# Performance work log

Measured on AMD Instinct MI355X. Metric: run time of the kernel, lower is better.

The kernel has to match this reference:

```python
import jax, jax.numpy as jnp
import numpy as np

BN_EPS = 1e-5
NUM_ROUTING_ITERS = 3


def _bn(x, gamma, beta, axes):
    # training-mode batch norm (torch default train mode): batch statistics
    mean = x.mean(axes, keepdims=True)
    var = x.var(axes, keepdims=True)
    return (x - mean) * jax.lax.rsqrt(var + BN_EPS) * gamma + beta


def _squash(x):
    # squash over last dim: sn * x / ((1+sn) * sqrt(sn))
    sn = jnp.sum(x * x, axis=-1, keepdims=True)
    return sn * x / ((1.0 + sn) * jnp.sqrt(sn))


def setup_inputs() -> dict:
    key = jax.random.key(0)
    ks = jax.random.split(key, 16)
    B, N = 4, 2048          # batch, num_points
    P, Q = 1024, 16         # prim_caps_size, prim_vec_size
    L, V = 64, 64           # latent_caps_size, latent_vec_size
    OUT = 40
    s = 0.02
    return {
        "x": jax.random.normal(ks[0], (B, 3, N), dtype=jnp.float32),
        # ConvLayer
        "w1": jax.random.normal(ks[1], (64, 3), dtype=jnp.float32) * s,
        "b1": jnp.zeros((64,), jnp.float32),
        "g1": jnp.ones((64,), jnp.float32),
        "be1": jnp.zeros((64,), jnp.float32),
        "w2": jax.random.normal(ks[2], (128, 64), dtype=jnp.float32) * s,
        "b2": jnp.zeros((128,), jnp.float32),
        "g2": jnp.ones((128,), jnp.float32),
        "be2": jnp.zeros((128,), jnp.float32),
        # PrimaryPointCapsLayer: Q parallel conv1d(128->P, k=1)+BN branches, stacked
        "w3": jax.random.normal(ks[3], (Q, P, 128), dtype=jnp.float32) * s,
        "b3": jnp.zeros((Q, P), jnp.float32),
        "g3": jnp.ones((Q, P), jnp.float32),
        "be3": jnp.zeros((Q, P), jnp.float32),
        # LatentCapsLayer routing weights
        "Wr": jax.random.normal(ks[4], (L, P, V, Q), dtype=jnp.float32) * 0.01,
        # classifier head
        "fc_w": jax.random.normal(ks[5], (OUT, L * V), dtype=jnp.float32) * s,
        "fc_b": jnp.zeros((OUT,), jnp.float32),
    }


def reference(x, w1, b1, g1, be1, w2, b2, g2, be2, w3, b3, g3, be3, Wr, fc_w, fc_b):
    B = x.shape[0]
    # ConvLayer: two 1x1 conv1d + BN + ReLU
    h = jnp.einsum("oc,bcn->bon", w1, x) + b1[None, :, None]
    h = jax.nn.relu(_bn(h, g1[None, :, None], be1[None, :, None], (0, 2)))
    h = jnp.einsum("oc,bcn->bon", w2, h) + b2[None, :, None]
    h = jax.nn.relu(_bn(h, g2[None, :, None], be2[None, :, None], (0, 2)))  # [B,128,N]

    # PrimaryPointCapsLayer: Q branches of conv1d+BN+global maxpool, vectorized
    u = jnp.einsum("qpc,bcn->bqpn", w3, h) + b3[None, :, :, None]  # [B,Q,P,N]
    u = _bn(u, g3[None, :, :, None], be3[None, :, :, None], (0, 3))
    u = u.max(axis=-1)                      # global maxpool -> [B,Q,P]
    u = jnp.transpose(u, (0, 2, 1))         # stack dim=2 in torch -> [B,P,Q]
    u = _squash(u)                          # squash over prim_vec

    # LatentCapsLayer dynamic routing
    u_hat = jnp.einsum("lpvq,bpq->blpv", Wr, u)   # [B,L,P,V]
    u_hat_d = jax.lax.stop_gradient(u_hat)
    L, P = Wr.shape[0], Wr.shape[1]
    b_ij = jnp.zeros((B, L, P), u_hat.dtype)
    for _ in range(NUM_ROUTING_ITERS - 1):
        c_ij = jax.nn.softmax(b_ij, axis=1)
        v_j = _squash(jnp.einsum("blp,blpv->blv", c_ij, u_hat_d))
        b_ij = b_ij + jnp.einsum("blv,blpv->blp", v_j, u_hat_d)
    c_ij = jax.nn.softmax(b_ij, axis=1)
    v_j = _squash(jnp.einsum("blp,blpv->blv", c_ij, u_hat))  # [B,L,V]

    presence = jnp.linalg.norm(v_j, axis=2)                   # [B,L]
    logits = v_j.reshape(B, -1) @ fc_w.T + fc_b               # [B,OUT]
    return (logits, presence)
```

## Files before the change

### kernel.cpp

```cpp
#include <hip/hip_runtime.h>
#include <math.h>

#define BN_EPS 1e-5f

typedef __attribute__((ext_vector_type(8))) _Float16 half8;
typedef __attribute__((ext_vector_type(4))) _Float16 half4;
typedef __attribute__((ext_vector_type(4))) float f32x4;
#define SPLIT_S  2048.0f
#define INV_S    (1.0f/2048.0f)

__global__ __launch_bounds__(256) void k_conv1stats(const float* __restrict__ x,
        const float* __restrict__ w1, float* __restrict__ y1,
        float* __restrict__ mean, float* __restrict__ inv) {
    const int o = blockIdx.x, t = threadIdx.x;
    const float wa = w1[o*3+0], wb = w1[o*3+1], wc = w1[o*3+2];
    float s = 0.f, ss = 0.f;
#pragma unroll
    for (int it = 0; it < 8; ++it) {
        int i = it * 256 + t;
        int b = i >> 9, n4 = (i & 511) * 4;
        const float* xb = x + (size_t)b * 6144 + n4;
        float4 x0 = *(const float4*)(xb);
        float4 x1 = *(const float4*)(xb + 2048);
        float4 x2 = *(const float4*)(xb + 4096);
        float4 r;
        r.x = wa*x0.x + wb*x1.x + wc*x2.x;
        r.y = wa*x0.y + wb*x1.y + wc*x2.y;
        r.z = wa*x0.z + wb*x1.z + wc*x2.z;
        r.w = wa*x0.w + wb*x1.w + wc*x2.w;
        *(float4*)(y1 + o * 8192 + i * 4) = r;
        s += r.x + r.y + r.z + r.w;
        ss = fmaf(r.x, r.x, fmaf(r.y, r.y, fmaf(r.z, r.z, fmaf(r.w, r.w, ss))));
    }
    __shared__ float rs[256], rss[256];
    rs[t] = s; rss[t] = ss;
    __syncthreads();
    for (int off = 128; off > 0; off >>= 1) {
        if (t < off) { rs[t] += rs[t+off]; rss[t] += rss[t+off]; }
        __syncthreads();
    }
    if (t == 0) {
        float m = rs[0] * (1.f/8192.f);
        float var = rss[0] * (1.f/8192.f) - m*m;
        mean[o] = m;
        inv[o]  = rsqrtf(var + BN_EPS);
    }
}

__global__ void k_stats(const float* __restrict__ y, float* __restrict__ mean,
                        float* __restrict__ inv) {
    int c = blockIdx.x, t = threadIdx.x;
    float s = 0.f, ss = 0.f;
    const float4* src = (const float4*)(y + c * 8192);
    for (int i = t; i < 2048; i += 256) {
        float4 v = src[i];
        s += v.x + v.y + v.z + v.w;
        ss = fmaf(v.x, v.x, fmaf(v.y, v.y, fmaf(v.z, v.z, fmaf(v.w, v.w, ss))));
    }
    __shared__ float rs[256], rss[256];
    rs[t] = s; rss[t] = ss;
    __syncthreads();
    for (int off = 128; off > 0; off >>= 1) {
        if (t < off) { rs[t] += rs[t+off]; rss[t] += rss[t+off]; }
        __syncthreads();
    }
    if (t == 0) {
        float m = rs[0] * (1.f/8192.f);
        float var = rss[0] * (1.f/8192.f) - m*m;
        mean[c] = m;
        inv[c]  = rsqrtf(var + BN_EPS);
    }
}

__global__ __launch_bounds__(256) void k_conv2(const float* __restrict__ y1,
        const float* __restrict__ w2,
        const float* __restrict__ mean1, const float* __restrict__ inv1,
        const float* __restrict__ g1, const float* __restrict__ be1,
        float* __restrict__ y2) {
    __shared__ float sc1[64], sh1[64];
    const int t = threadIdx.x;
    if (t < 64) {
        float sc = inv1[t] * g1[t];
        sc1[t] = sc;
        sh1[t] = be1[t] - mean1[t] * sc;
    }
    __syncthreads();
    int bn0 = (blockIdx.x * 256 + t) * 4;
    int og0 = blockIdx.y * 4;
    float4 acc[4];
#pragma unroll
    for (int j = 0; j < 4; ++j) acc[j] = float4{0.f,0.f,0.f,0.f};
    for (int c = 0; c < 64; ++c) {
        float4 hv = *(const float4*)(y1 + c*8192 + bn0);
        float sc = sc1[c], sh = sh1[c];
        hv.x = fmaxf(fmaf(hv.x, sc, sh), 0.f);
        hv.y = fmaxf(fmaf(hv.y, sc, sh), 0.f);
        hv.z = fmaxf(fmaf(hv.z, sc, sh), 0.f);
        hv.w = fmaxf(fmaf(hv.w, sc, sh), 0.f);
#pragma unroll
        for (int j = 0; j < 4; ++j) {
            float w = w2[(og0+j)*64 + c];
            acc[j].x = fmaf(w, hv.x, acc[j].x); acc[j].y = fmaf(w, hv.y, acc[j].y);
            acc[j].z = fmaf(w, hv.z, acc[j].z); acc[j].w = fmaf(w, hv.w, acc[j].w);
        }
    }
#pragma unroll
    for (int j = 0; j < 4; ++j) *(float4*)(y2 + (og0+j)*8192 + bn0) = acc[j];
}

__global__ void k_split_w3(const float* __restrict__ w, const float* __restrict__ g3,
                           _Float16* __restrict__ hi, _Float16* __restrict__ lo) {
    int base = blockIdx.x * 256 + threadIdx.x;
#pragma unroll
    for (int it = 0; it < 4; ++it) {
        int i = (base + it * 131072) * 4;
        float4 d = *reinterpret_cast<const float4*>(w + i);
        float sgn = (g3[i >> 7] < 0.f) ? -1.f : 1.f;
        float vs[4] = {d.x * sgn, d.y * sgn, d.z * sgn, d.w * sgn};
        half4 h4, l4;
#pragma unroll
        for (int j = 0; j < 4; ++j) {
            _Float16 h = (_Float16)vs[j];
            h4[j] = h;
            l4[j] = (_Float16)((vs[j] - (float)h) * SPLIT_S);
        }
        *reinterpret_cast<half4*>(hi + i) = h4;
        *reinterpret_cast<half4*>(lo + i) = l4;
    }
}

__global__ __launch_bounds__(256) void k_h2t_split(const float* __restrict__ y2,
        const float* __restrict__ mean, const float* __restrict__ inv,
        const float* __restrict__ g, const float* __restrict__ be,
        _Float16* __restrict__ hi, _Float16* __restrict__ lo) {
    __shared__ float tile[64][65];
    const int t = threadIdx.x;
    const int bn0 = blockIdx.x * 64, c0 = blockIdx.y * 64;
#pragma unroll
    for (int r = 0; r < 4; ++r) {
        int idx = r * 256 + t;
        int cl = idx >> 4, bn4 = (idx & 15) * 4;
        int c = c0 + cl;
        float sc = inv[c] * g[c];
        float sh = be[c] - mean[c] * sc;
        float4 d = *(const float4*)(y2 + (size_t)c * 8192 + bn0 + bn4);
        tile[cl][bn4  ] = fmaxf(fmaf(d.x, sc, sh), 0.f);
        tile[cl][bn4+1] = fmaxf(fmaf(d.y, sc, sh), 0.f);
        tile[cl][bn4+2] = fmaxf(fmaf(d.z, sc, sh), 0.f);
        tile[cl][bn4+3] = fmaxf(fmaf(d.w, sc, sh), 0.f);
    }
    __syncthreads();
#pragma unroll
    for (int r = 0; r < 4; ++r) {
        int idx = r * 256 + t;
        int bnl = idx >> 4, c4 = (idx & 15) * 4;
        half4 h4, l4;
#pragma unroll
        for (int j = 0; j < 4; ++j) {
            float v = tile[c4 + j][bnl];
            _Float16 h = (_Float16)v;
            h4[j] = h;
            l4[j] = (_Float16)((v - (float)h) * SPLIT_S);
        }
        size_t o = (size_t)(bn0 + bnl) * 128 + c0 + c4;
        *reinterpret_cast<half4*>(hi + o) = h4;
        *reinterpret_cast<half4*>(lo + o) = l4;
    }
}

__global__ __launch_bounds__(256, 2) void k_caps(
        const _Float16* __restrict__ w3h, const _Float16* __restrict__ w3l,
        const _Float16* __restrict__ h2h, const _Float16* __restrict__ h2l,
        float* __restrict__ umax,
        float* __restrict__ usum_b, float* __restrict__ usumsq_b) {
    const int lane = threadIdx.x & 63, wave = threadIdx.x >> 6;
    const int b = blockIdx.y;
    const int mrow = blockIdx.x * 128 + wave * 32;
    const int r16 = lane & 15, kq = lane >> 4;

    __shared__ _Float16 Bs[2][2][8][64][8];

    half8 Ah[2][4], Al[2][4];
#pragma unroll
    for (int mt = 0; mt < 2; ++mt) {
        const size_t base = (size_t)(mrow + mt*16 + r16) * 128 + kq * 8;
#pragma unroll
        for (int ks = 0; ks < 4; ++ks) {
            Ah[mt][ks] = *reinterpret_cast<const half8*>(w3h + base + ks*32);
            Al[mt][ks] = *reinterpret_cast<const half8*>(w3l + base + ks*32);
        }
    }
    float mx[2][4], sm[2][4], sq[2][4];
#pragma unroll
    for (int mt = 0; mt < 2; ++mt)
#pragma unroll
        for (int r = 0; r < 4; ++r) {
            mx[mt][r] = -3.4e38f; sm[mt][r] = 0.f; sq[mt][r] = 0.f;
        }

    const int u0 = wave * 2;
    const size_t srow = (size_t)(b*2048 + r16) * 128 + wave * 32 + kq * 8;

    {
#pragma unroll
        for (int g = 0; g < 2; ++g) {
            const size_t a = srow + (size_t)g * 16 * 128;
            *reinterpret_cast<half8*>(&Bs[0][g][u0  ][lane][0]) = *reinterpret_cast<const half8*>(h2h + a);
            *reinterpret_cast<half8*>(&Bs[0][g][u0+1][lane][0]) = *reinterpret_cast<const half8*>(h2l + a);
        }
    }
    __syncthreads();

    for (int nt = 0; nt < 64; ++nt) {
        const int buf = nt & 1;
        const int ntn = (nt + 1 < 64) ? nt + 1 : nt;
        const size_t snext = srow + (size_t)ntn * 32 * 128;
        half8 g0h = *reinterpret_cast<const half8*>(h2h + snext);
        half8 g0l = *reinterpret_cast<const half8*>(h2l + snext);
        half8 g1h = *reinterpret_cast<const half8*>(h2h + snext + 2048);
        half8 g1l = *reinterpret_cast<const half8*>(h2l + snext + 2048);

#pragma unroll
        for (int g = 0; g < 2; ++g) {
            f32x4 acc[2], accx[2];
#pragma unroll
            for (int mt = 0; mt < 2; ++mt) { acc[mt] = f32x4{0.f,0.f,0.f,0.f}; accx[mt] = f32x4{0.f,0.f,0.f,0.f}; }
#pragma unroll
            for (int ks = 0; ks < 4; ++ks) {
                half8 Bh = *reinterpret_cast<const half8*>(&Bs[buf][g][ks*2  ][lane][0]);
                half8 Bl = *reinterpret_cast<const half8*>(&Bs[buf][g][ks*2+1][lane][0]);
#pragma unroll
                for (int mt = 0; mt < 2; ++mt) {
                    acc[mt]  = __builtin_amdgcn_mfma_f32_16x16x32_f16(Ah[mt][ks], Bh, acc[mt], 0, 0, 0);
                    accx[mt] = __builtin_amdgcn_mfma_f32_16x16x32_f16(Ah[mt][ks], Bl, accx[mt], 0, 0, 0);
                    accx[mt] = __builtin_amdgcn_mfma_f32_16x16x32_f16(Al[mt][ks], Bh, accx[mt], 0, 0, 0);
                }
            }
#pragma unroll
            for (int mt = 0; mt < 2; ++mt)
#pragma unroll
                for (int r = 0; r < 4; ++r) {
                    float v = fmaf(accx[mt][r], INV_S, acc[mt][r]);
                    mx[mt][r] = fmaxf(mx[mt][r], v);
                    sm[mt][r] += v;
                    sq[mt][r] = fmaf(v, v, sq[mt][r]);
                }
        }
        *reinterpret_cast<half8*>(&Bs[buf^1][0][u0  ][lane][0]) = g0h;
        *reinterpret_cast<half8*>(&Bs[buf^1][0][u0+1][lane][0]) = g0l;
        *reinterpret_cast<half8*>(&Bs[buf^1][1][u0  ][lane][0]) = g1h;
        *reinterpret_cast<half8*>(&Bs[buf^1][1][u0+1][lane][0]) = g1l;
        __syncthreads();
    }

#pragma unroll
    for (int off = 8; off >= 1; off >>= 1)
#pragma unroll
        for (int mt = 0; mt < 2; ++mt)
#pragma unroll
            for (int r = 0; r < 4; ++r) {
                mx[mt][r] = fmaxf(mx[mt][r], __shfl_xor(mx[mt][r], off));
                sm[mt][r] += __shfl_xor(sm[mt][r], off);
                sq[mt][r] += __shfl_xor(sq[mt][r], off);
            }
    if (r16 == 0) {
#pragma unroll
        for (int mt = 0; mt < 2; ++mt)
#pragma unroll
            for (int r = 0; r < 4; ++r) {
                int qp = mrow + mt*16 + kq*4 + r;
                umax[b*16384 + qp]     = mx[mt][r];
                usum_b[b*16384 + qp]   = sm[mt][r];
                usumsq_b[b*16384 + qp] = sq[mt][r];
            }
    }
}

__global__ void k_u(const float* __restrict__ umax,
                    const float* __restrict__ usum_b, const float* __restrict__ usumsq_b,
                    const float* __restrict__ g3, const float* __restrict__ be3,
                    float* __restrict__ u) {
    int tg = blockIdx.x * 256 + threadIdx.x;
    int b = tg >> 10, p = tg & 1023;
    float ub[16]; float sn = 0.f;
#pragma unroll
    for (int q = 0; q < 16; ++q) {
        int qp = q * 1024 + p;
        float s  = usum_b[qp] + usum_b[16384+qp] + usum_b[32768+qp] + usum_b[49152+qp];
        float ss = usumsq_b[qp] + usumsq_b[16384+qp] + usumsq_b[32768+qp] + usumsq_b[49152+qp];
        float g  = g3[qp];
        float sgn = (g < 0.f) ? -1.f : 1.f;
        float mean  = sgn * s * (1.f/8192.f);
        float var   = ss * (1.f/8192.f) - mean*mean;
        float scale = g * rsqrtf(var + BN_EPS);
        float val = sgn * umax[b*16384 + qp];
        float vb = (val - mean) * scale + be3[qp];
        ub[q] = vb; sn = fmaf(vb, vb, sn);
    }
    float f = sqrtf(sn) / (1.f + sn);
#pragma unroll
    for (int q = 0; q < 16; ++q) u[tg*16 + q] = ub[q] * f;
}

__global__ __launch_bounds__(256) void k_uhat(const float* __restrict__ Wr,
                                              const float* __restrict__ u,
                                              float* __restrict__ uhat2,
                                              float* __restrict__ s1p) {
    const int t = threadIdx.x;
    const int pblk = blockIdx.x, l = blockIdx.y;
    __shared__ float wr[4][64][20];
    __shared__ float us[4][4][16];
    const int bb = t >> 6, v = t & 63;
    float s1acc = 0.f;
    for (int sub = 0; sub < 8; ++sub) {
        const int p0 = pblk * 32 + sub * 4;
        const float* src = Wr + ((size_t)l * 1024 + p0) * 1024;
        if (sub) __syncthreads();
#pragma unroll
        for (int it = 0; it < 4; ++it) {
            float4 d = *(const float4*)(src + (it*256 + t) * 4);
            int vv = t >> 2, q0 = (t & 3) * 4;
            *(float4*)&wr[it][vv][q0] = d;
        }
        {
            int p = t >> 6, b2 = (t >> 4) & 3, q = t & 15;
            us[p][b2][q] = u[((size_t)b2 * 1024 + p0 + p) * 16 + q];
        }
        __syncthreads();
#pragma unroll
        for (int p = 0; p < 4; ++p) {
            float acc = 0.f;
#pragma unroll
            for (int q4 = 0; q4 < 4; ++q4) {
                float4 wf = *(const float4*)&wr[p][v][q4*4];
                float4 uf = *(const float4*)&us[p][bb][q4*4];
                acc = fmaf(wf.x, uf.x, acc);
                acc = fmaf(wf.y, uf.y, acc);
                acc = fmaf(wf.z, uf.z, acc);
                acc = fmaf(wf.w, uf.w, acc);
            }
            uhat2[(((size_t)bb * 1024 + p0 + p) * 64 + l) * 64 + v] = acc;
            s1acc += acc;
        }
    }
    s1p[(((size_t)pblk * 4 + bb) * 64 + l) * 64 + v] = s1acc;
}

__global__ void k_s1red(const float* __restrict__ s1p, float* __restrict__ vout) {
    const int wv = blockIdx.x;
    const int b = wv >> 6, l = wv & 63;
    const int v = threadIdx.x;
    float acc = 0.f;
#pragma unroll
    for (int pblk = 0; pblk < 32; ++pblk)
        acc += s1p[(((size_t)pblk * 4 + b) * 64 + l) * 64 + v];
    float s = acc * (1.f/64.f);
    float sn = s * s;
#pragma unroll
    for (int off = 32; off >= 1; off >>= 1) sn += __shfl_xor(sn, off);
    vout[wv * 64 + v] = s * sqrtf(sn) / (1.f + sn);
}

__global__ __launch_bounds__(256) void k_route(const float* __restrict__ uhat2,
                                               const float* __restrict__ vin,
                                               float* __restrict__ bij,
                                               float* __restrict__ part, const int read_b) {
    const int blk = blockIdx.x;
    const int b = blk >> 7, ch = blk & 127;
    const int p0 = ch * 8;
    const int t = threadIdx.x;
    const int v = t & 63, w = t >> 6;
    __shared__ float uh[64][68];
    __shared__ float vs[64][68];
    __shared__ float bl[64];
    {
        const float* src = vin + b * 4096;
        for (int i = t; i < 1024; i += 256) {
            float4 d = *(const float4*)(src + i * 4);
            int l = i >> 4, v0 = (i & 15) * 4;
            vs[l][v0] = d.x; vs[l][v0+1] = d.y; vs[l][v0+2] = d.z; vs[l][v0+3] = d.w;
        }
    }
    float sacc[16];
#pragma unroll
    for (int j = 0; j < 16; ++j) sacc[j] = 0.f;

    for (int pp = 0; pp < 8; ++pp) {
        const int p = p0 + pp;
        __syncthreads();
        const float* src = uhat2 + ((size_t)b * 1024 + p) * 4096;
        for (int i = t; i < 1024; i += 256) {
            float4 d = *(const float4*)(src + i * 4);
            int l = i >> 4, v0 = (i & 15) * 4;
            uh[l][v0] = d.x; uh[l][v0+1] = d.y; uh[l][v0+2] = d.z; uh[l][v0+3] = d.w;
        }
        __syncthreads();
#pragma unroll
        for (int i = 0; i < 16; ++i) {
            const int l = w * 16 + i;
            float prod = uh[l][v] * vs[l][v];
#pragma unroll
            for (int off = 32; off >= 1; off >>= 1) prod += __shfl_xor(prod, off);
            if (v == 0) {
                float bb = prod;
                if (read_b) bb += bij[(b * 64 + l) * 1024 + p];
                bl[l] = bb;
                if (!read_b) bij[(b * 64 + l) * 1024 + p] = bb;
            }
        }
        __syncthreads();
        float xv = bl[v];
        float m = xv;
#pragma unroll
        for (int off = 32; off >= 1; off >>= 1) m = fmaxf(m, __shfl_xor(m, off));
        float e = expf(xv - m);
        float sgm = e;
#pragma unroll
        for (int off = 32; off >= 1; off >>= 1) sgm += __shfl_xor(sgm, off);
        float c = e / sgm;
#pragma unroll
        for (int j = 0; j < 16; ++j) {
            const int l = j * 4 + w;
            float cl = __shfl(c, l);
            sacc[j] = fmaf(cl, uh[l][v], sacc[j]);
        }
    }
#pragma unroll
    for (int j = 0; j < 16; ++j) {
        const int l = j * 4 + w;
        part[((size_t)(b * 128 + ch) * 64 + l) * 64 + v] = sacc[j];
    }
}

__global__ void k_red_squash(const float* __restrict__ part, float* __restrict__ vout,
                             float* __restrict__ pres) {
    const int wv = blockIdx.x;
    const int b = wv >> 6, l = wv & 63;
    const int v = threadIdx.x;
    float acc = 0.f;
    for (int ch = 0; ch < 128; ++ch) acc += part[((size_t)(b * 128 + ch) * 64 + l) * 64 + v];
    float sn = acc * acc;
#pragma unroll
    for (int off = 32; off >= 1; off >>= 1) sn += __shfl_xor(sn, off);
    vout[wv * 64 + v] = acc * sqrtf(sn) / (1.f + sn);
    if (pres != nullptr && v == 0) pres[wv] = sn / (1.f + sn);
}

__global__ void k_logits(const float* __restrict__ vj, const float* __restrict__ fcw,
                         const float* __restrict__ fcb, float* __restrict__ out) {
    int wv = blockIdx.x * 4 + (threadIdx.x >> 6);
    int lane = threadIdx.x & 63;
    int b = wv / 40, o = wv % 40;
    const float* xv = vj + b * 4096;
    const float* wr = fcw + (size_t)o * 4096;
    float acc = 0.f;
    for (int i = lane; i < 4096; i += 64) acc = fmaf(xv[i], wr[i], acc);
#pragma unroll
    for (int off = 32; off >= 1; off >>= 1) acc += __shfl_xor(acc, off);
    if (lane == 0) out[b * 40 + o] = acc + fcb[o];
}

extern "C" void kernel_launch(void* const* d_in, const int* in_sizes, int n_in,
                              void* d_out, int out_size, void* d_ws, size_t ws_size,
                              hipStream_t stream) {
    const float* x   = (const float*)d_in[0];
    const float* w1  = (const float*)d_in[1];
    const float* g1  = (const float*)d_in[3];
    const float* be1 = (const float*)d_in[4];
    const float* w2  = (const float*)d_in[5];
    const float* g2  = (const float*)d_in[7];
    const float* be2 = (const float*)d_in[8];
    const float* w3  = (const float*)d_in[9];
    const float* g3  = (const float*)d_in[11];
    const float* be3 = (const float*)d_in[12];
    const float* Wr  = (const float*)d_in[13];
    const float* fcw = (const float*)d_in[14];
    const float* fcb = (const float*)d_in[15];
    float* out = (float*)d_out;

    float* ws       = (float*)d_ws;
    float* y1       = ws;
    float* y2       = y1 + 524288;
    float* mean1    = y2 + 1048576;
    float* inv1     = mean1 + 64;
    float* mean2    = inv1 + 64;
    float* inv2     = mean2 + 128;
    float* umax     = inv2 + 128;
    float* usum_b   = umax + 65536;
    float* usumsq_b = usum_b + 65536;
    float* u        = usumsq_b + 65536;
    float* v1       = u + 65536;
    float* v2       = v1 + 16384;
    float* vj       = v2 + 16384;
    float* bij      = vj + 16384;
    float* s1p      = bij + 262144;
    float* part     = s1p + 524288;
    float* uhat2    = part + 2097152;
    _Float16* w3h = (_Float16*)uhat2;
    _Float16* w3l = w3h + 2097152;
    _Float16* h2h = w3l + 2097152;
    _Float16* h2l = h2h + 1048576;

    k_conv1stats<<<64, 256, 0, stream>>>(x, w1, y1, mean1, inv1);
    k_conv2<<<dim3(8, 32), 256, 0, stream>>>(y1, w2, mean1, inv1, g1, be1, y2);
    k_stats<<<128, 256, 0, stream>>>(y2, mean2, inv2);
    k_split_w3<<<512, 256, 0, stream>>>(w3, g3, w3h, w3l);
    k_h2t_split<<<dim3(128, 2), 256, 0, stream>>>(y2, mean2, inv2, g2, be2, h2h, h2l);
    k_caps<<<dim3(128, 4), 256, 0, stream>>>(w3h, w3l, h2h, h2l, umax, usum_b, usumsq_b);
    k_u<<<16, 256, 0, stream>>>(umax, usum_b, usumsq_b, g3, be3, u);
    k_uhat<<<dim3(32, 64), 256, 0, stream>>>(Wr, u, uhat2, s1p);
    k_s1red<<<256, 64, 0, stream>>>(s1p, v1);
    k_route<<<512, 256, 0, stream>>>(uhat2, v1, bij, part, 0);
    k_red_squash<<<256, 64, 0, stream>>>(part, v2, nullptr);
    k_route<<<512, 256, 0, stream>>>(uhat2, v2, bij, part, 1);
    k_red_squash<<<256, 64, 0, stream>>>(part, vj, out + 160);
    k_logits<<<40, 256, 0, stream>>>(vj, fcw, fcb, out);
}
```

Baseline: 692.4 us.

## Fuse w3 split into conv1, shrink caps tile, fold k_u into k_uhat

The w3 fp16 hi/lo split now runs as extra blocks inside the first conv/stats kernel, and the per-capsule BN+squash kernel is folded into k_uhat, where each block recomputes its 32 capsules into shared memory. This removes two launches. k_caps now gives each wave one 16-row M tile instead of two, doubling the grid and raising the occupancy hint to 4 blocks per SM. In exchange, every B tile staged in LDS is reused by half as many MFMAs, and the k_u work is repeated across the 64 l-blocks in k_uhat.

After: 725.6 us. 4.8% more time.

```diff
diff --git a/kernel.cpp b/kernel.cpp
--- a/kernel.cpp
+++ b/kernel.cpp
@@ -9,10 +9,34 @@
 #define SPLIT_S  2048.0f
 #define INV_S    (1.0f/2048.0f)
 
-__global__ __launch_bounds__(256) void k_conv1stats(const float* __restrict__ x,
+
+__global__ __launch_bounds__(256) void k_pre(const float* __restrict__ x,
         const float* __restrict__ w1, float* __restrict__ y1,
-        float* __restrict__ mean, float* __restrict__ inv) {
-    const int o = blockIdx.x, t = threadIdx.x;
+        float* __restrict__ mean, float* __restrict__ inv,
+        const float* __restrict__ w3, const float* __restrict__ g3,
+        _Float16* __restrict__ hi, _Float16* __restrict__ lo) {
+    const int t = threadIdx.x;
+    if (blockIdx.x < 512) {
+        int base = blockIdx.x * 256 + t;
+#pragma unroll
+        for (int it = 0; it < 4; ++it) {
+            int i = (base + it * 131072) * 4;
+            float4 d = *reinterpret_cast<const float4*>(w3 + i);
+            float sgn = (g3[i >> 7] < 0.f) ? -1.f : 1.f;
+            float vs[4] = {d.x * sgn, d.y * sgn, d.z * sgn, d.w * sgn};
+            half4 h4, l4;
+#pragma unroll
+            for (int j = 0; j < 4; ++j) {
+                _Float16 h = (_Float16)vs[j];
+                h4[j] = h;
+                l4[j] = (_Float16)((vs[j] - (float)h) * SPLIT_S);
+            }
+            *reinterpret_cast<half4*>(hi + i) = h4;
+            *reinterpret_cast<half4*>(lo + i) = l4;
+        }
+        return;
+    }
+    const int o = blockIdx.x - 512;
     const float wa = w1[o*3+0], wb = w1[o*3+1], wc = w1[o*3+2];
     float s = 0.f, ss = 0.f;
 #pragma unroll
@@ -108,27 +132,6 @@
     for (int j = 0; j < 4; ++j) *(float4*)(y2 + (og0+j)*8192 + bn0) = acc[j];
 }
 
-__global__ void k_split_w3(const float* __restrict__ w, const float* __restrict__ g3,
-                           _Float16* __restrict__ hi, _Float16* __restrict__ lo) {
-    int base = blockIdx.x * 256 + threadIdx.x;
-#pragma unroll
-    for (int it = 0; it < 4; ++it) {
-        int i = (base + it * 131072) * 4;
-        float4 d = *reinterpret_cast<const float4*>(w + i);
-        float sgn = (g3[i >> 7] < 0.f) ? -1.f : 1.f;
-        float vs[4] = {d.x * sgn, d.y * sgn, d.z * sgn, d.w * sgn};
-        half4 h4, l4;
-#pragma unroll
-        for (int j = 0; j < 4; ++j) {
-            _Float16 h = (_Float16)vs[j];
-            h4[j] = h;
-            l4[j] = (_Float16)((vs[j] - (float)h) * SPLIT_S);
-        }
-        *reinterpret_cast<half4*>(hi + i) = h4;
-        *reinterpret_cast<half4*>(lo + i) = l4;
-    }
-}
-
 __global__ __launch_bounds__(256) void k_h2t_split(const float* __restrict__ y2,
         const float* __restrict__ mean, const float* __restrict__ inv,
         const float* __restrict__ g, const float* __restrict__ be,
@@ -168,35 +171,28 @@
     }
 }
 
-__global__ __launch_bounds__(256, 2) void k_caps(
+__global__ __launch_bounds__(256, 4) void k_caps(
         const _Float16* __restrict__ w3h, const _Float16* __restrict__ w3l,
         const _Float16* __restrict__ h2h, const _Float16* __restrict__ h2l,
         float* __restrict__ umax,
         float* __restrict__ usum_b, float* __restrict__ usumsq_b) {
     const int lane = threadIdx.x & 63, wave = threadIdx.x >> 6;
     const int b = blockIdx.y;
-    const int mrow = blockIdx.x * 128 + wave * 32;
+    const int mrow = blockIdx.x * 64 + wave * 16;
     const int r16 = lane & 15, kq = lane >> 4;
 
     __shared__ _Float16 Bs[2][2][8][64][8];
 
-    half8 Ah[2][4], Al[2][4];
-#pragma unroll
-    for (int mt = 0; mt < 2; ++mt) {
-        const size_t base = (size_t)(mrow + mt*16 + r16) * 128 + kq * 8;
-#pragma unroll
-        for (int ks = 0; ks < 4; ++ks) {
-            Ah[mt][ks] = *reinterpret_cast<const half8*>(w3h + base + ks*32);
-            Al[mt][ks] = *reinterpret_cast<const half8*>(w3l + base + ks*32);
-        }
-    }
-    float mx[2][4], sm[2][4], sq[2][4];
-#pragma unroll
-    for (int mt = 0; mt < 2; ++mt)
-#pragma unroll
-        for (int r = 0; r < 4; ++r) {
-            mx[mt][r] = -3.4e38f; sm[mt][r] = 0.f; sq[mt][r] = 0.f;
-        }
+    half8 Ah[4], Al[4];
+    const size_t abase = (size_t)(mrow + r16) * 128 + kq * 8;
+#pragma unroll
+    for (int ks = 0; ks < 4; ++ks) {
+        Ah[ks] = *reinterpret_cast<const half8*>(w3h + abase + ks*32);
+        Al[ks] = *reinterpret_cast<const half8*>(w3l + abase + ks*32);
+    }
+    float mx[4], sm[4], sq[4];
+#pragma unroll
+    for (int r = 0; r < 4; ++r) { mx[r] = -3.4e38f; sm[r] = 0.f; sq[r] = 0.f; }
 
     const int u0 = wave * 2;
     const size_t srow = (size_t)(b*2048 + r16) * 128 + wave * 32 + kq * 8;
@@ -222,29 +218,23 @@
 
 #pragma unroll
         for (int g = 0; g < 2; ++g) {
-            f32x4 acc[2], accx[2];
-#pragma unroll
-            for (int mt = 0; mt < 2; ++mt) { acc[mt] = f32x4{0.f,0.f,0.f,0.f}; accx[mt] = f32x4{0.f,0.f,0.f,0.f}; }
+            f32x4 acc = f32x4{0.f,0.f,0.f,0.f};
+            f32x4 accx = f32x4{0.f,0.f,0.f,0.f};
 #pragma unroll
             for (int ks = 0; ks < 4; ++ks) {
                 half8 Bh = *reinterpret_cast<const half8*>(&Bs[buf][g][ks*2  ][lane][0]);
                 half8 Bl = *reinterpret_cast<const half8*>(&Bs[buf][g][ks*2+1][lane][0]);
-#pragma unroll
-                for (int mt = 0; mt < 2; ++mt) {
-                    acc[mt]  = __builtin_amdgcn_mfma_f32_16x16x32_f16(Ah[mt][ks], Bh, acc[mt], 0, 0, 0);
-                    accx[mt] = __builtin_amdgcn_mfma_f32_16x16x32_f16(Ah[mt][ks], Bl, accx[mt], 0, 0, 0);
-                    accx[mt] = __builtin_amdgcn_mfma_f32_16x16x32_f16(Al[mt][ks], Bh, accx[mt], 0, 0, 0);
-                }
+                acc  = __builtin_amdgcn_mfma_f32_16x16x32_f16(Ah[ks], Bh, acc, 0, 0, 0);
+                accx = __builtin_amdgcn_mfma_f32_16x16x32_f16(Ah[ks], Bl, accx, 0, 0, 0);
+                accx = __builtin_amdgcn_mfma_f32_16x16x32_f16(Al[ks], Bh, accx, 0, 0, 0);
             }
 #pragma unroll
-            for (int mt = 0; mt < 2; ++mt)
-#pragma unroll
-                for (int r = 0; r < 4; ++r) {
-                    float v = fmaf(accx[mt][r], INV_S, acc[mt][r]);
-                    mx[mt][r] = fmaxf(mx[mt][r], v);
-                    sm[mt][r] += v;
-                    sq[mt][r] = fmaf(v, v, sq[mt][r]);
-                }
+            for (int r = 0; r < 4; ++r) {
+                float v = fmaf(accx[r], INV_S, acc[r]);
+                mx[r] = fmaxf(mx[r], v);
+                sm[r] += v;
+                sq[r] = fmaf(v, v, sq[r]);
+            }
         }
         *reinterpret_cast<half8*>(&Bs[buf^1][0][u0  ][lane][0]) = g0h;
         *reinterpret_cast<half8*>(&Bs[buf^1][0][u0+1][lane][0]) = g0l;
@@ -256,61 +246,59 @@
 #pragma unroll
     for (int off = 8; off >= 1; off >>= 1)
 #pragma unroll
-        for (int mt = 0; mt < 2; ++mt)
-#pragma unroll
-            for (int r = 0; r < 4; ++r) {
-                mx[mt][r] = fmaxf(mx[mt][r], __shfl_xor(mx[mt][r], off));
-                sm[mt][r] += __shfl_xor(sm[mt][r], off);
-                sq[mt][r] += __shfl_xor(sq[mt][r], off);
-            }
+        for (int r = 0; r < 4; ++r) {
+            mx[r] = fmaxf(mx[r], __shfl_xor(mx[r], off));
+            sm[r] += __shfl_xor(sm[r], off);
+            sq[r] += __shfl_xor(sq[r], off);
+        }
     if (r16 == 0) {
 #pragma unroll
-        for (int mt = 0; mt < 2; ++mt)
-#pragma unroll
-            for (int r = 0; r < 4; ++r) {
-                int qp = mrow + mt*16 + kq*4 + r;
-                umax[b*16384 + qp]     = mx[mt][r];
-                usum_b[b*16384 + qp]   = sm[mt][r];
-                usumsq_b[b*16384 + qp] = sq[mt][r];
-            }
-    }
-}
-
-__global__ void k_u(const float* __restrict__ umax,
-                    const float* __restrict__ usum_b, const float* __restrict__ usumsq_b,
-                    const float* __restrict__ g3, const float* __restrict__ be3,
-                    float* __restrict__ u) {
-    int tg = blockIdx.x * 256 + threadIdx.x;
-    int b = tg >> 10, p = tg & 1023;
-    float ub[16]; float sn = 0.f;
-#pragma unroll
-    for (int q = 0; q < 16; ++q) {
-        int qp = q * 1024 + p;
-        float s  = usum_b[qp] + usum_b[16384+qp] + usum_b[32768+qp] + usum_b[49152+qp];
-        float ss = usumsq_b[qp] + usumsq_b[16384+qp] + usumsq_b[32768+qp] + usumsq_b[49152+qp];
-        float g  = g3[qp];
-        float sgn = (g < 0.f) ? -1.f : 1.f;
-        float mean  = sgn * s * (1.f/8192.f);
-        float var   = ss * (1.f/8192.f) - mean*mean;
-        float scale = g * rsqrtf(var + BN_EPS);
-        float val = sgn * umax[b*16384 + qp];
-        float vb = (val - mean) * scale + be3[qp];
-        ub[q] = vb; sn = fmaf(vb, vb, sn);
-    }
-    float f = sqrtf(sn) / (1.f + sn);
-#pragma unroll
-    for (int q = 0; q < 16; ++q) u[tg*16 + q] = ub[q] * f;
+        for (int r = 0; r < 4; ++r) {
+            int qp = mrow + kq*4 + r;
+            umax[b*16384 + qp]     = mx[r];
+            usum_b[b*16384 + qp]   = sm[r];
+            usumsq_b[b*16384 + qp] = sq[r];
+        }
+    }
 }
 
 __global__ __launch_bounds__(256) void k_uhat(const float* __restrict__ Wr,
-                                              const float* __restrict__ u,
+                                              const float* __restrict__ umax,
+                                              const float* __restrict__ usum_b,
+                                              const float* __restrict__ usumsq_b,
+                                              const float* __restrict__ g3,
+                                              const float* __restrict__ be3,
                                               float* __restrict__ uhat2,
                                               float* __restrict__ s1p) {
     const int t = threadIdx.x;
     const int pblk = blockIdx.x, l = blockIdx.y;
     __shared__ float wr[4][64][20];
-    __shared__ float us[4][4][16];
+    __shared__ float us_all[32][4][16];
     const int bb = t >> 6, v = t & 63;
+
+    if (t < 128) {
+        int p = t & 31, b2 = t >> 5;
+        int pg = pblk * 32 + p;
+        float ub[16]; float sn = 0.f;
+#pragma unroll
+        for (int q = 0; q < 16; ++q) {
+            int qp = q * 1024 + pg;
+            float s  = usum_b[qp] + usum_b[16384+qp] + usum_b[32768+qp] + usum_b[49152+qp];
+            float ss = usumsq_b[qp] + usumsq_b[16384+qp] + usumsq_b[32768+qp] + usumsq_b[49152+qp];
+            float g  = g3[qp];
+            float sgn = (g < 0.f) ? -1.f : 1.f;
+            float mean  = sgn * s * (1.f/8192.f);
+            float var   = ss * (1.f/8192.f) - mean*mean;
+            float scale = g * rsqrtf(var + BN_EPS);
+            float val = sgn * umax[b2*16384 + qp];
+            float vb = (val - mean) * scale + be3[qp];
+            ub[q] = vb; sn = fmaf(vb, vb, sn);
+        }
+        float f = sqrtf(sn) / (1.f + sn);
+#pragma unroll
+        for (int q = 0; q < 16; ++q) us_all[p][b2][q] = ub[q] * f;
+    }
+
     float s1acc = 0.f;
     for (int sub = 0; sub < 8; ++sub) {
         const int p0 = pblk * 32 + sub * 4;
@@ -322,18 +310,15 @@
             int vv = t >> 2, q0 = (t & 3) * 4;
             *(float4*)&wr[it][vv][q0] = d;
         }
-        {
-            int p = t >> 6, b2 = (t >> 4) & 3, q = t & 15;
-            us[p][b2][q] = u[((size_t)b2 * 1024 + p0 + p) * 16 + q];
-        }
         __syncthreads();
 #pragma unroll
         for (int p = 0; p < 4; ++p) {
             float acc = 0.f;
+            const int pl = sub * 4 + p;
 #pragma unroll
             for (int q4 = 0; q4 < 4; ++q4) {
                 float4 wf = *(const float4*)&wr[p][v][q4*4];
-                float4 uf = *(const float4*)&us[p][bb][q4*4];
+                float4 uf = *(const float4*)&us_all[pl][bb][q4*4];
                 acc = fmaf(wf.x, uf.x, acc);
                 acc = fmaf(wf.y, uf.y, acc);
                 acc = fmaf(wf.z, uf.z, acc);
@@ -488,8 +473,8 @@
     float* umax     = inv2 + 128;
     float* usum_b   = umax + 65536;
     float* usumsq_b = usum_b + 65536;
-    float* u        = usumsq_b + 65536;
-    float* v1       = u + 65536;
+    float* u_unused = usumsq_b + 65536;
+    float* v1       = u_unused + 65536;
     float* v2       = v1 + 16384;
     float* vj       = v2 + 16384;
     float* bij      = vj + 16384;
@@ -501,14 +486,12 @@
     _Float16* h2h = w3l + 2097152;
     _Float16* h2l = h2h + 1048576;
 
-    k_conv1stats<<<64, 256, 0, stream>>>(x, w1, y1, mean1, inv1);
+    k_pre<<<576, 256, 0, stream>>>(x, w1, y1, mean1, inv1, w3, g3, w3h, w3l);
     k_conv2<<<dim3(8, 32), 256, 0, stream>>>(y1, w2, mean1, inv1, g1, be1, y2);
     k_stats<<<128, 256, 0, stream>>>(y2, mean2, inv2);
-    k_split_w3<<<512, 256, 0, stream>>>(w3, g3, w3h, w3l);
     k_h2t_split<<<dim3(128, 2), 256, 0, stream>>>(y2, mean2, inv2, g2, be2, h2h, h2l);
-    k_caps<<<dim3(128, 4), 256, 0, stream>>>(w3h, w3l, h2h, h2l, umax, usum_b, usumsq_b);
-    k_u<<<16, 256, 0, stream>>>(umax, usum_b, usumsq_b, g3, be3, u);
-    k_uhat<<<dim3(32, 64), 256, 0, stream>>>(Wr, u, uhat2, s1p);
+    k_caps<<<dim3(256, 4), 256, 0, stream>>>(w3h, w3l, h2h, h2l, umax, usum_b, usumsq_b);
+    k_uhat<<<dim3(32, 64), 256, 0, stream>>>(Wr, umax, usum_b, usumsq_b, g3, be3, uhat2, s1p);
     k_s1red<<<256, 64, 0, stream>>>(s1p, v1);
     k_route<<<512, 256, 0, stream>>>(uhat2, v1, bij, part, 0);
     k_red_squash<<<256, 64, 0, stream>>>(part, v2, nullptr);
```
